# Performance work log

Hardware: AMD Instinct MI355X
Metric: run time of the kernel (lower is better)

The kernel has to match this reference:

```python
import jax, jax.numpy as jnp
import numpy as np

THRESHOLD = 0.5
DECAY = 0.2


def setup_inputs() -> dict:
    key = jax.random.key(0)
    ks = jax.random.split(key, 5)
    B, D_IN, D_H, D_OUT = 4096, 1024, 4096, 1024
    x = jax.random.normal(ks[0], (B, D_IN), dtype=jnp.float32)
    W1 = jax.random.normal(ks[1], (D_H, D_IN), dtype=jnp.float32) * (1.0 / np.sqrt(D_IN))
    b1 = jax.random.normal(ks[2], (D_H,), dtype=jnp.float32) * 0.01
    W2 = jax.random.normal(ks[3], (D_OUT, D_H), dtype=jnp.float32) * (1.0 / np.sqrt(D_H))
    b2 = jax.random.normal(ks[4], (D_OUT,), dtype=jnp.float32) * 0.01
    return {"x": x, "W1": W1, "b1": b1, "W2": W2, "b2": b2, "time_steps": 100}


def reference(x, W1, b1, W2, b2, time_steps):
    B = x.shape[0]
    D_OUT = W2.shape[0]
    mem0 = jnp.zeros((B, D_OUT), dtype=x.dtype)
    spike0 = jnp.zeros((B, D_OUT), dtype=x.dtype)

    def step(carry, _):
        xt, mem, spike = carry
        h = jax.nn.relu(xt @ W1.T + b1)        # [B, D_H]
        y = h @ W2.T + b2                       # [B, D_OUT]; note: x is overwritten each step
        mem = mem * DECAY + y
        s = (mem >= THRESHOLD).astype(xt.dtype)
        mem = mem * (1.0 - s)                   # reset fired neurons
        return (y, mem, spike + s), None

    (_, _, spike), _ = jax.lax.scan(step, (x, mem0, spike0), None, length=time_steps)
    return spike / time_steps
```

## Files before the change

### kernel.cpp

```cpp
#include <hip/hip_runtime.h>
#include <cstddef>

constexpr int BB     = 4096;
constexpr int DIN    = 1024;
constexpr int DH     = 4096;
constexpr int DOUT   = 1024;
constexpr int TSTEPS = 100;
constexpr float DECAYC  = 0.2f;
constexpr float THRESHC = 0.5f;

template<int EPI>
__global__ __launch_bounds__(256, 3)
void sgemm_nt(const float* __restrict__ A, const float* __restrict__ Bm,
              const float* __restrict__ bias, float* __restrict__ C,
              int M, int N, int K, int kLen,
              float* __restrict__ memv, float* __restrict__ spike,
              float* __restrict__ ynext)
{
    __shared__ float As[16][132];
    __shared__ float Bs[16][132];

    int bx = blockIdx.x, by = blockIdx.y;
    {
        const int nwg = gridDim.x * gridDim.y;
        if ((nwg & 7) == 0) {
            const int id  = by * gridDim.x + bx;
            const int cpx = nwg >> 3;
            const int nid = (id & 7) * cpx + (id >> 3);
            bx = nid % gridDim.x;
            by = nid / gridDim.x;
        }
    }

    const int tid  = threadIdx.x;
    const int row0 = bx * 128;
    const int col0 = by * 128;
    const int k0   = blockIdx.z * kLen;

    const int sr = tid >> 2;
    const int sk = (tid & 3) << 2;
    const int tx = tid & 15;
    const int ty = tid >> 4;

    float acc[8][8];
#pragma unroll
    for (int i = 0; i < 8; ++i)
#pragma unroll
        for (int j = 0; j < 8; ++j) acc[i][j] = 0.f;

    const float* Ag = A  + (size_t)(row0 + sr) * K + k0 + sk;
    const float* Bg = Bm + (size_t)(col0 + sr) * K + k0 + sk;
    const size_t step64 = (size_t)64 * K;

    const int nt = kLen >> 4;

    float4 a0 = *(const float4*)(Ag);
    float4 a1 = *(const float4*)(Ag + step64);
    float4 b0 = *(const float4*)(Bg);
    float4 b1 = *(const float4*)(Bg + step64);

    for (int kt = 0; kt < nt; ++kt) {
        __syncthreads();
        As[sk+0][sr]    = a0.x; As[sk+1][sr]    = a0.y; As[sk+2][sr]    = a0.z; As[sk+3][sr]    = a0.w;
        As[sk+0][sr+64] = a1.x; As[sk+1][sr+64] = a1.y; As[sk+2][sr+64] = a1.z; As[sk+3][sr+64] = a1.w;
        Bs[sk+0][sr]    = b0.x; Bs[sk+1][sr]    = b0.y; Bs[sk+2][sr]    = b0.z; Bs[sk+3][sr]    = b0.w;
        Bs[sk+0][sr+64] = b1.x; Bs[sk+1][sr+64] = b1.y; Bs[sk+2][sr+64] = b1.z; Bs[sk+3][sr+64] = b1.w;
        __syncthreads();

        if (kt + 1 < nt) {
            Ag += 16; Bg += 16;
            a0 = *(const float4*)(Ag);
            a1 = *(const float4*)(Ag + step64);
            b0 = *(const float4*)(Bg);
            b1 = *(const float4*)(Bg + step64);
        }

#pragma unroll
        for (int k = 0; k < 16; ++k) {
            float4 av0 = *(const float4*)&As[k][ty*4];
            float4 av1 = *(const float4*)&As[k][ty*4 + 64];
            float4 bv0 = *(const float4*)&Bs[k][tx*4];
            float4 bv1 = *(const float4*)&Bs[k][tx*4 + 64];
            float a[8] = {av0.x, av0.y, av0.z, av0.w, av1.x, av1.y, av1.z, av1.w};
            float b[8] = {bv0.x, bv0.y, bv0.z, bv0.w, bv1.x, bv1.y, bv1.z, bv1.w};
#pragma unroll
            for (int i = 0; i < 8; ++i)
#pragma unroll
                for (int j = 0; j < 8; ++j)
                    acc[i][j] = fmaf(a[i], b[j], acc[i][j]);
        }
    }

#pragma unroll
    for (int ih = 0; ih < 2; ++ih) {
#pragma unroll
        for (int i4 = 0; i4 < 4; ++i4) {
            const int i = ih * 4 + i4;
            const int r = row0 + ty * 4 + ih * 64 + i4;
#pragma unroll
            for (int jh = 0; jh < 2; ++jh) {
                const int c = col0 + tx * 4 + jh * 64;
                const size_t idx = (size_t)r * N + c;
                if constexpr (EPI == 0) {
                    const float4 bv = *(const float4*)(bias + c);
                    float4 v;
                    v.x = acc[i][jh*4+0] + bv.x;
                    v.y = acc[i][jh*4+1] + bv.y;
                    v.z = acc[i][jh*4+2] + bv.z;
                    v.w = acc[i][jh*4+3] + bv.w;
                    v.x = v.x > 0.f ? v.x : 0.f;
                    v.y = v.y > 0.f ? v.y : 0.f;
                    v.z = v.z > 0.f ? v.z : 0.f;
                    v.w = v.w > 0.f ? v.w : 0.f;
                    *(float4*)(C + idx) = v;
                } else if constexpr (EPI == 1) {
                    float4 v;
                    v.x = acc[i][jh*4+0];
                    v.y = acc[i][jh*4+1];
                    v.z = acc[i][jh*4+2];
                    v.w = acc[i][jh*4+3];
                    *(float4*)(C + (size_t)blockIdx.z * M * N + idx) = v;
                } else {
                    const float4 bv = *(const float4*)(bias + c);
                    float4 mv = *(const float4*)(memv + idx);
                    float4 sv = *(const float4*)(spike + idx);
                    float4 yv;
#define SNN_STEP(comp, aval)                                            \
                    { float y = (aval) + bv.comp;                       \
                      float m = mv.comp * DECAYC + y;                   \
                      float sf = (m >= THRESHC) ? 1.f : 0.f;            \
                      mv.comp = (m >= THRESHC) ? 0.f : m;               \
                      sv.comp += sf;                                    \
                      yv.comp = y; }
                    SNN_STEP(x, acc[i][jh*4+0])
                    SNN_STEP(y, acc[i][jh*4+1])
                    SNN_STEP(z, acc[i][jh*4+2])
                    SNN_STEP(w, acc[i][jh*4+3])
#undef SNN_STEP
                    *(float4*)(ynext + idx) = yv;
                    *(float4*)(memv  + idx) = mv;
                    *(float4*)(spike + idx) = sv;
                }
            }
        }
    }
}

__global__ __launch_bounds__(256)
void reduce_epi(const float* __restrict__ part, const float* __restrict__ b2,
                float* __restrict__ memv, float* __restrict__ spike,
                float* __restrict__ ynext)
{
    const size_t MN4 = (size_t)BB * DOUT / 4;
    const size_t i = (size_t)blockIdx.x * 256 + threadIdx.x;
    const float4* p = (const float4*)part;
    const float4 p0 = p[i];
    const float4 p1 = p[i + MN4];
    const float4 p2 = p[i + 2 * MN4];
    const float4 p3 = p[i + 3 * MN4];
    const int colv = (int)(i & (DOUT / 4 - 1));
    const float4 bv = ((const float4*)b2)[colv];
    float4 mv = ((float4*)memv)[i];
    float4 sv = ((float4*)spike)[i];
    float4 yv;
#define SNN_RED(comp)                                                   \
    { float y = (((p0.comp + p1.comp) + p2.comp) + p3.comp) + bv.comp;  \
      float m = mv.comp * DECAYC + y;                                   \
      float sf = (m >= THRESHC) ? 1.f : 0.f;                            \
      mv.comp = (m >= THRESHC) ? 0.f : m;                               \
      sv.comp += sf;                                                    \
      yv.comp = y; }
    SNN_RED(x) SNN_RED(y) SNN_RED(z) SNN_RED(w)
#undef SNN_RED
    ((float4*)ynext)[i] = yv;
    ((float4*)memv)[i]  = mv;
    ((float4*)spike)[i] = sv;
}

__global__ __launch_bounds__(256)
void scale_out(float* __restrict__ out)
{
    const size_t i = (size_t)blockIdx.x * 256 + threadIdx.x;
    float4 v = ((float4*)out)[i];
    v.x /= (float)TSTEPS; v.y /= (float)TSTEPS;
    v.z /= (float)TSTEPS; v.w /= (float)TSTEPS;
    ((float4*)out)[i] = v;
}

extern "C" void kernel_launch(void* const* d_in, const int* in_sizes, int n_in,
                              void* d_out, int out_size, void* d_ws, size_t ws_size,
                              hipStream_t stream)
{
    const float* x  = (const float*)d_in[0];
    const float* W1 = (const float*)d_in[1];
    const float* b1 = (const float*)d_in[2];
    const float* W2 = (const float*)d_in[3];
    const float* b2 = (const float*)d_in[4];
    float* out = (float*)d_out;

    const size_t MN = (size_t)BB * DOUT;
    const size_t MH = (size_t)BB * DH;
    float* ws   = (float*)d_ws;
    float* xcur = ws;
    float* h    = xcur + MN;
    float* memv = h + MH;
    float* part = memv + MN;
    const size_t need_full = (MN + MH + MN + 4 * MN) * sizeof(float);
    const bool use_splitk = ws_size >= need_full;

    (void)hipMemsetAsync(memv, 0, MN * sizeof(float), stream);
    (void)hipMemsetAsync(out,  0, MN * sizeof(float), stream);

    const dim3 blk(256);
    const dim3 g1(BB / 128, DH / 128, 1);
    const dim3 g2s(BB / 128, DOUT / 128, 4);
    const dim3 g2f(BB / 128, DOUT / 128, 1);
    const dim3 ge(MN / 4 / 256);

    for (int t = 0; t < TSTEPS; ++t) {
        const float* xin = (t == 0) ? x : xcur;
        sgemm_nt<0><<<g1, blk, 0, stream>>>(xin, W1, b1, h,
                                            BB, DH, DIN, DIN,
                                            nullptr, nullptr, nullptr);
        if (use_splitk) {
            sgemm_nt<1><<<g2s, blk, 0, stream>>>(h, W2, nullptr, part,
                                                 BB, DOUT, DH, DH / 4,
                                                 nullptr, nullptr, nullptr);
            reduce_epi<<<ge, blk, 0, stream>>>(part, b2, memv, out, xcur);
        } else {
            sgemm_nt<2><<<g2f, blk, 0, stream>>>(h, W2, b2, nullptr,
                                                 BB, DOUT, DH, DH,
                                                 memv, out, xcur);
        }
    }
    scale_out<<<ge, blk, 0, stream>>>(out);
}
```

Measured before the change: 78.97 ms.

## Skip GEMMs once the recurrent input stops changing and widen the N tile to 256

Each step's epilogue compares the new y against the previous y and sets a per-step flag if any element changed. The next step's GEMM kernels return early when that flag is zero, so after the iteration reaches a fixed point only the cheap reduce/epilogue runs. Separately, the GEMM tile grows from 128x128 to 128x256 per block (8x16 accumulators, occupancy lowered to 2), and B is now loaded as one 16-wide row per thread. Skipping is exact only if y truly repeats bit-for-bit. The wider tile raises register pressure, and the uncoalesced B load layout may hurt bandwidth.

```diff
diff --git a/kernel.cpp b/kernel.cpp
--- a/kernel.cpp
+++ b/kernel.cpp
@@ -10,15 +10,18 @@
 constexpr float THRESHC = 0.5f;
 
 template<int EPI>
-__global__ __launch_bounds__(256, 3)
+__global__ __launch_bounds__(256, 2)
 void sgemm_nt(const float* __restrict__ A, const float* __restrict__ Bm,
               const float* __restrict__ bias, float* __restrict__ C,
               int M, int N, int K, int kLen,
               float* __restrict__ memv, float* __restrict__ spike,
-              float* __restrict__ ynext)
-{
+              float* __restrict__ ynext,
+              const int* __restrict__ skipFlag, int* __restrict__ setFlag)
+{
+    if (skipFlag != nullptr && *skipFlag == 0) return;
+
     __shared__ float As[16][132];
-    __shared__ float Bs[16][132];
+    __shared__ float Bs[16][260];
 
     int bx = blockIdx.x, by = blockIdx.y;
     {
@@ -34,45 +37,50 @@
 
     const int tid  = threadIdx.x;
     const int row0 = bx * 128;
-    const int col0 = by * 128;
+    const int col0 = by * 256;
     const int k0   = blockIdx.z * kLen;
 
-    const int sr = tid >> 2;
-    const int sk = (tid & 3) << 2;
-    const int tx = tid & 15;
-    const int ty = tid >> 4;
-
-    float acc[8][8];
+    const int sra = tid >> 1;
+    const int ska = (tid & 1) << 3;
+    const int tx  = tid & 15;
+    const int ty  = tid >> 4;
+
+    float acc[8][16];
 #pragma unroll
     for (int i = 0; i < 8; ++i)
 #pragma unroll
-        for (int j = 0; j < 8; ++j) acc[i][j] = 0.f;
-
-    const float* Ag = A  + (size_t)(row0 + sr) * K + k0 + sk;
-    const float* Bg = Bm + (size_t)(col0 + sr) * K + k0 + sk;
-    const size_t step64 = (size_t)64 * K;
+        for (int j = 0; j < 16; ++j) acc[i][j] = 0.f;
+
+    const float* Ag = A  + (size_t)(row0 + sra) * K + k0 + ska;
+    const float* Bg = Bm + (size_t)(col0 + tid) * K + k0;
 
     const int nt = kLen >> 4;
 
     float4 a0 = *(const float4*)(Ag);
-    float4 a1 = *(const float4*)(Ag + step64);
+    float4 a1 = *(const float4*)(Ag + 4);
     float4 b0 = *(const float4*)(Bg);
-    float4 b1 = *(const float4*)(Bg + step64);
+    float4 b1 = *(const float4*)(Bg + 4);
+    float4 b2v = *(const float4*)(Bg + 8);
+    float4 b3 = *(const float4*)(Bg + 12);
 
     for (int kt = 0; kt < nt; ++kt) {
         __syncthreads();
-        As[sk+0][sr]    = a0.x; As[sk+1][sr]    = a0.y; As[sk+2][sr]    = a0.z; As[sk+3][sr]    = a0.w;
-        As[sk+0][sr+64] = a1.x; As[sk+1][sr+64] = a1.y; As[sk+2][sr+64] = a1.z; As[sk+3][sr+64] = a1.w;
-        Bs[sk+0][sr]    = b0.x; Bs[sk+1][sr]    = b0.y; Bs[sk+2][sr]    = b0.z; Bs[sk+3][sr]    = b0.w;
-        Bs[sk+0][sr+64] = b1.x; Bs[sk+1][sr+64] = b1.y; Bs[sk+2][sr+64] = b1.z; Bs[sk+3][sr+64] = b1.w;
+        As[ska+0][sra] = a0.x; As[ska+1][sra] = a0.y; As[ska+2][sra] = a0.z; As[ska+3][sra] = a0.w;
+        As[ska+4][sra] = a1.x; As[ska+5][sra] = a1.y; As[ska+6][sra] = a1.z; As[ska+7][sra] = a1.w;
+        Bs[ 0][tid] = b0.x;  Bs[ 1][tid] = b0.y;  Bs[ 2][tid] = b0.z;  Bs[ 3][tid] = b0.w;
+        Bs[ 4][tid] = b1.x;  Bs[ 5][tid] = b1.y;  Bs[ 6][tid] = b1.z;  Bs[ 7][tid] = b1.w;
+        Bs[ 8][tid] = b2v.x; Bs[ 9][tid] = b2v.y; Bs[10][tid] = b2v.z; Bs[11][tid] = b2v.w;
+        Bs[12][tid] = b3.x;  Bs[13][tid] = b3.y;  Bs[14][tid] = b3.z;  Bs[15][tid] = b3.w;
         __syncthreads();
 
         if (kt + 1 < nt) {
             Ag += 16; Bg += 16;
-            a0 = *(const float4*)(Ag);
-            a1 = *(const float4*)(Ag + step64);
-            b0 = *(const float4*)(Bg);
-            b1 = *(const float4*)(Bg + step64);
+            a0  = *(const float4*)(Ag);
+            a1  = *(const float4*)(Ag + 4);
+            b0  = *(const float4*)(Bg);
+            b1  = *(const float4*)(Bg + 4);
+            b2v = *(const float4*)(Bg + 8);
+            b3  = *(const float4*)(Bg + 12);
         }
 
 #pragma unroll
@@ -81,12 +89,15 @@
             float4 av1 = *(const float4*)&As[k][ty*4 + 64];
             float4 bv0 = *(const float4*)&Bs[k][tx*4];
             float4 bv1 = *(const float4*)&Bs[k][tx*4 + 64];
-            float a[8] = {av0.x, av0.y, av0.z, av0.w, av1.x, av1.y, av1.z, av1.w};
-            float b[8] = {bv0.x, bv0.y, bv0.z, bv0.w, bv1.x, bv1.y, bv1.z, bv1.w};
+            float4 bv2 = *(const float4*)&Bs[k][tx*4 + 128];
+            float4 bv3 = *(const float4*)&Bs[k][tx*4 + 192];
+            float a[8]  = {av0.x, av0.y, av0.z, av0.w, av1.x, av1.y, av1.z, av1.w};
+            float b[16] = {bv0.x, bv0.y, bv0.z, bv0.w, bv1.x, bv1.y, bv1.z, bv1.w,
+                           bv2.x, bv2.y, bv2.z, bv2.w, bv3.x, bv3.y, bv3.z, bv3.w};
 #pragma unroll
             for (int i = 0; i < 8; ++i)
 #pragma unroll
-                for (int j = 0; j < 8; ++j)
+                for (int j = 0; j < 16; ++j)
                     acc[i][j] = fmaf(a[i], b[j], acc[i][j]);
         }
     }
@@ -98,7 +109,7 @@
             const int i = ih * 4 + i4;
             const int r = row0 + ty * 4 + ih * 64 + i4;
 #pragma unroll
-            for (int jh = 0; jh < 2; ++jh) {
+            for (int jh = 0; jh < 4; ++jh) {
                 const int c = col0 + tx * 4 + jh * 64;
                 const size_t idx = (size_t)r * N + c;
                 if constexpr (EPI == 0) {
@@ -124,6 +135,7 @@
                     const float4 bv = *(const float4*)(bias + c);
                     float4 mv = *(const float4*)(memv + idx);
                     float4 sv = *(const float4*)(spike + idx);
+                    const float4 oldv = *(const float4*)(ynext + idx);
                     float4 yv;
 #define SNN_STEP(comp, aval)                                            \
                     { float y = (aval) + bv.comp;                       \
@@ -137,6 +149,8 @@
                     SNN_STEP(z, acc[i][jh*4+2])
                     SNN_STEP(w, acc[i][jh*4+3])
 #undef SNN_STEP
+                    if (yv.x != oldv.x || yv.y != oldv.y ||
+                        yv.z != oldv.z || yv.w != oldv.w) *setFlag = 1;
                     *(float4*)(ynext + idx) = yv;
                     *(float4*)(memv  + idx) = mv;
                     *(float4*)(spike + idx) = sv;
@@ -149,7 +163,7 @@
 __global__ __launch_bounds__(256)
 void reduce_epi(const float* __restrict__ part, const float* __restrict__ b2,
                 float* __restrict__ memv, float* __restrict__ spike,
-                float* __restrict__ ynext)
+                float* __restrict__ ynext, int* __restrict__ setFlag)
 {
     const size_t MN4 = (size_t)BB * DOUT / 4;
     const size_t i = (size_t)blockIdx.x * 256 + threadIdx.x;
@@ -162,6 +176,7 @@
     const float4 bv = ((const float4*)b2)[colv];
     float4 mv = ((float4*)memv)[i];
     float4 sv = ((float4*)spike)[i];
+    const float4 oldv = ((float4*)ynext)[i];
     float4 yv;
 #define SNN_RED(comp)                                                   \
     { float y = (((p0.comp + p1.comp) + p2.comp) + p3.comp) + bv.comp;  \
@@ -172,6 +187,8 @@
       yv.comp = y; }
     SNN_RED(x) SNN_RED(y) SNN_RED(z) SNN_RED(w)
 #undef SNN_RED
+    if (yv.x != oldv.x || yv.y != oldv.y ||
+        yv.z != oldv.z || yv.w != oldv.w) *setFlag = 1;
     ((float4*)ynext)[i] = yv;
     ((float4*)memv)[i]  = mv;
     ((float4*)spike)[i] = sv;
@@ -200,37 +217,44 @@
 
     const size_t MN = (size_t)BB * DOUT;
     const size_t MH = (size_t)BB * DH;
-    float* ws   = (float*)d_ws;
-    float* xcur = ws;
-    float* h    = xcur + MN;
-    float* memv = h + MH;
-    float* part = memv + MN;
-    const size_t need_full = (MN + MH + MN + 4 * MN) * sizeof(float);
+    float* ws    = (float*)d_ws;
+    float* xcur  = ws;
+    float* h     = xcur + MN;
+    float* memv  = h + MH;
+    int*   flags = (int*)(memv + MN);
+    float* part  = (float*)(flags + 128);
+    const size_t need_full = (MN + MH + MN + 4 * MN) * sizeof(float) + 512;
     const bool use_splitk = ws_size >= need_full;
 
-    (void)hipMemsetAsync(memv, 0, MN * sizeof(float), stream);
-    (void)hipMemsetAsync(out,  0, MN * sizeof(float), stream);
+    (void)hipMemsetAsync(memv,  0, MN * sizeof(float), stream);
+    (void)hipMemsetAsync(out,   0, MN * sizeof(float), stream);
+    (void)hipMemsetAsync(flags, 0, TSTEPS * sizeof(int), stream);
 
     const dim3 blk(256);
-    const dim3 g1(BB / 128, DH / 128, 1);
-    const dim3 g2s(BB / 128, DOUT / 128, 4);
-    const dim3 g2f(BB / 128, DOUT / 128, 1);
+    const dim3 g1(BB / 128, DH / 256, 1);
+    const dim3 g2s(BB / 128, DOUT / 256, 4);
+    const dim3 g2f(BB / 128, DOUT / 256, 1);
     const dim3 ge(MN / 4 / 256);
 
     for (int t = 0; t < TSTEPS; ++t) {
         const float* xin = (t == 0) ? x : xcur;
+        const int* skip = (t > 0) ? (flags + t - 1) : nullptr;
         sgemm_nt<0><<<g1, blk, 0, stream>>>(xin, W1, b1, h,
                                             BB, DH, DIN, DIN,
-                                            nullptr, nullptr, nullptr);
+                                            nullptr, nullptr, nullptr,
+                                            skip, nullptr);
         if (use_splitk) {
             sgemm_nt<1><<<g2s, blk, 0, stream>>>(h, W2, nullptr, part,
                                                  BB, DOUT, DH, DH / 4,
-                                                 nullptr, nullptr, nullptr);
-            reduce_epi<<<ge, blk, 0, stream>>>(part, b2, memv, out, xcur);
+                                                 nullptr, nullptr, nullptr,
+                                                 skip, nullptr);
+            reduce_epi<<<ge, blk, 0, stream>>>(part, b2, memv, out, xcur,
+                                               flags + t);
         } else {
             sgemm_nt<2><<<g2f, blk, 0, stream>>>(h, W2, b2, nullptr,
                                                  BB, DOUT, DH, DH,
-                                                 memv, out, xcur);
+                                                 memv, out, xcur,
+                                                 skip, flags + t);
         }
     }
     scale_out<<<ge, blk, 0, stream>>>(out);
```

New measurement: 101.3 ms. +28.3%, slower.

## Widen SGEMM block tile to 128x256 with 8x16 per-thread micro-tile

Applied to the files above, without the earlier changes.

Doubles the N dimension of each block tile to 256 columns and each thread's accumulator to 8x16, raising arithmetic intensity per shared-memory load. It also drops the register prefetch of the next K-tile: global loads now happen at the top of each iteration, right before the barrier. Launch bounds fall to 2 waves per SIMD to make room for the larger accumulator. The risks are register pressure or spills, lower occupancy, exposed global load latency, and fewer blocks in the grid.

```diff
diff --git a/kernel.cpp b/kernel.cpp
--- a/kernel.cpp
+++ b/kernel.cpp
@@ -10,7 +10,7 @@
 constexpr float THRESHC = 0.5f;
 
 template<int EPI>
-__global__ __launch_bounds__(256, 3)
+__global__ __launch_bounds__(256, 2)
 void sgemm_nt(const float* __restrict__ A, const float* __restrict__ Bm,
               const float* __restrict__ bias, float* __restrict__ C,
               int M, int N, int K, int kLen,
@@ -18,7 +18,7 @@
               float* __restrict__ ynext)
 {
     __shared__ float As[16][132];
-    __shared__ float Bs[16][132];
+    __shared__ float Bs[16][260];
 
     int bx = blockIdx.x, by = blockIdx.y;
     {
@@ -34,46 +34,45 @@
 
     const int tid  = threadIdx.x;
     const int row0 = bx * 128;
-    const int col0 = by * 128;
+    const int col0 = by * 256;
     const int k0   = blockIdx.z * kLen;
 
-    const int sr = tid >> 2;
-    const int sk = (tid & 3) << 2;
+    const int sr = tid >> 1;
+    const int sk = (tid & 1) << 3;
     const int tx = tid & 15;
     const int ty = tid >> 4;
 
-    float acc[8][8];
+    float acc[8][16];
 #pragma unroll
     for (int i = 0; i < 8; ++i)
 #pragma unroll
-        for (int j = 0; j < 8; ++j) acc[i][j] = 0.f;
+        for (int j = 0; j < 16; ++j) acc[i][j] = 0.f;
 
     const float* Ag = A  + (size_t)(row0 + sr) * K + k0 + sk;
     const float* Bg = Bm + (size_t)(col0 + sr) * K + k0 + sk;
-    const size_t step64 = (size_t)64 * K;
+    const size_t step128 = (size_t)128 * K;
 
     const int nt = kLen >> 4;
 
-    float4 a0 = *(const float4*)(Ag);
-    float4 a1 = *(const float4*)(Ag + step64);
-    float4 b0 = *(const float4*)(Bg);
-    float4 b1 = *(const float4*)(Bg + step64);
-
     for (int kt = 0; kt < nt; ++kt) {
+        const float4 a0  = *(const float4*)(Ag);
+        const float4 a1  = *(const float4*)(Ag + 4);
+        const float4 b0  = *(const float4*)(Bg);
+        const float4 b1  = *(const float4*)(Bg + 4);
+        const float4 b2v = *(const float4*)(Bg + step128);
+        const float4 b3  = *(const float4*)(Bg + step128 + 4);
+        Ag += 16; Bg += 16;
+
         __syncthreads();
-        As[sk+0][sr]    = a0.x; As[sk+1][sr]    = a0.y; As[sk+2][sr]    = a0.z; As[sk+3][sr]    = a0.w;
-        As[sk+0][sr+64] = a1.x; As[sk+1][sr+64] = a1.y; As[sk+2][sr+64] = a1.z; As[sk+3][sr+64] = a1.w;
-        Bs[sk+0][sr]    = b0.x; Bs[sk+1][sr]    = b0.y; Bs[sk+2][sr]    = b0.z; Bs[sk+3][sr]    = b0.w;
-        Bs[sk+0][sr+64] = b1.x; Bs[sk+1][sr+64] = b1.y; Bs[sk+2][sr+64] = b1.z; Bs[sk+3][sr+64] = b1.w;
+        As[sk+0][sr] = a0.x; As[sk+1][sr] = a0.y; As[sk+2][sr] = a0.z; As[sk+3][sr] = a0.w;
+        As[sk+4][sr] = a1.x; As[sk+5][sr] = a1.y; As[sk+6][sr] = a1.z; As[sk+7][sr] = a1.w;
+        Bs[sk+0][sr] = b0.x; Bs[sk+1][sr] = b0.y; Bs[sk+2][sr] = b0.z; Bs[sk+3][sr] = b0.w;
+        Bs[sk+4][sr] = b1.x; Bs[sk+5][sr] = b1.y; Bs[sk+6][sr] = b1.z; Bs[sk+7][sr] = b1.w;
+        Bs[sk+0][sr+128] = b2v.x; Bs[sk+1][sr+128] = b2v.y;
+        Bs[sk+2][sr+128] = b2v.z; Bs[sk+3][sr+128] = b2v.w;
+        Bs[sk+4][sr+128] = b3.x;  Bs[sk+5][sr+128] = b3.y;
+        Bs[sk+6][sr+128] = b3.z;  Bs[sk+7][sr+128] = b3.w;
         __syncthreads();
-
-        if (kt + 1 < nt) {
-            Ag += 16; Bg += 16;
-            a0 = *(const float4*)(Ag);
-            a1 = *(const float4*)(Ag + step64);
-            b0 = *(const float4*)(Bg);
-            b1 = *(const float4*)(Bg + step64);
-        }
 
 #pragma unroll
         for (int k = 0; k < 16; ++k) {
@@ -81,12 +80,15 @@
             float4 av1 = *(const float4*)&As[k][ty*4 + 64];
             float4 bv0 = *(const float4*)&Bs[k][tx*4];
             float4 bv1 = *(const float4*)&Bs[k][tx*4 + 64];
-            float a[8] = {av0.x, av0.y, av0.z, av0.w, av1.x, av1.y, av1.z, av1.w};
-            float b[8] = {bv0.x, bv0.y, bv0.z, bv0.w, bv1.x, bv1.y, bv1.z, bv1.w};
+            float4 bv2 = *(const float4*)&Bs[k][tx*4 + 128];
+            float4 bv3 = *(const float4*)&Bs[k][tx*4 + 192];
+            float a[8]  = {av0.x, av0.y, av0.z, av0.w, av1.x, av1.y, av1.z, av1.w};
+            float b[16] = {bv0.x, bv0.y, bv0.z, bv0.w, bv1.x, bv1.y, bv1.z, bv1.w,
+                           bv2.x, bv2.y, bv2.z, bv2.w, bv3.x, bv3.y, bv3.z, bv3.w};
 #pragma unroll
             for (int i = 0; i < 8; ++i)
 #pragma unroll
-                for (int j = 0; j < 8; ++j)
+                for (int j = 0; j < 16; ++j)
                     acc[i][j] = fmaf(a[i], b[j], acc[i][j]);
         }
     }
@@ -98,7 +100,7 @@
             const int i = ih * 4 + i4;
             const int r = row0 + ty * 4 + ih * 64 + i4;
 #pragma unroll
-            for (int jh = 0; jh < 2; ++jh) {
+            for (int jh = 0; jh < 4; ++jh) {
                 const int c = col0 + tx * 4 + jh * 64;
                 const size_t idx = (size_t)r * N + c;
                 if constexpr (EPI == 0) {
@@ -212,9 +214,9 @@
     (void)hipMemsetAsync(out,  0, MN * sizeof(float), stream);
 
     const dim3 blk(256);
-    const dim3 g1(BB / 128, DH / 128, 1);
-    const dim3 g2s(BB / 128, DOUT / 128, 4);
-    const dim3 g2f(BB / 128, DOUT / 128, 1);
+    const dim3 g1(BB / 128, DH / 256, 1);
+    const dim3 g2s(BB / 128, DOUT / 256, 4);
+    const dim3 g2f(BB / 128, DOUT / 256, 1);
     const dim3 ge(MN / 4 / 256);
 
     for (int t = 0; t < TSTEPS; ++t) {
```

After: 92.72 ms. +17.4%, slower.
